# Performance work log

Hardware: AMD Instinct MI355X
Metric: run time of the kernel (lower is better)

## Reference

```python
import jax, jax.numpy as jnp
import numpy as np


def _gru(ub, lengths, W_ih, W_hh, b_ih, b_hh, h0):
    # ub: [B,T,E] pooled basket sequence; emulates packed GRU + pad_packed:
    # hidden carries forward only while t < length; outputs are zero past length.
    B, T, E = ub.shape
    x_t = jnp.transpose(ub, (1, 0, 2))                      # [T,B,E]
    mask_t = (jnp.arange(T)[:, None] < lengths[None, :])    # [T,B]
    xg_t = x_t @ W_ih.T + b_ih                              # [T,B,3E] precompute input gates

    def step(h, inp):
        xg, m = inp                                         # [B,3E], [B]
        hg = h @ W_hh.T + b_hh                              # [B,3E]
        xr, xz, xn = jnp.split(xg, 3, axis=-1)
        hr, hz, hn = jnp.split(hg, 3, axis=-1)
        r = jax.nn.sigmoid(xr + hr)
        z = jax.nn.sigmoid(xz + hz)
        n = jnp.tanh(xn + r * hn)
        h_new = (1.0 - z) * n + z * h
        m = m[:, None]
        h_next = jnp.where(m, h_new, h)
        out = jnp.where(m, h_new, 0.0)                      # pad_packed pads with zeros
        return h_next, out

    h_last, outs = jax.lax.scan(step, h0[0], (xg_t, mask_t))
    dynamic_user = jnp.transpose(outs, (1, 0, 2))           # [B,T,E]
    return dynamic_user, h_last[None]                        # h_u: [1,B,E]


def setup_inputs() -> dict:
    key = jax.random.key(0)
    B, T, M, E, V = 256, 50, 20, 128, 100000
    ks = jax.random.split(key, 8)
    basket_sizes = jax.random.randint(ks[0], (B, T), 1, M + 1)
    item_ids = jax.random.randint(ks[1], (B, T, M), 1, V + 2)
    pos = jnp.arange(M)
    item_ids = jnp.where(pos[None, None, :] < basket_sizes[..., None], item_ids, 0)
    lengths = jnp.sort(jax.random.randint(ks[2], (B,), 1, T + 1))[::-1]  # descending, like pack_padded
    emb = jax.random.normal(ks[3], (V + 2, E), jnp.float32) * 0.1
    emb = emb.at[0].set(0.0)                                 # padding_idx=0
    s = 1.0 / np.sqrt(E)
    W_ih = jax.random.uniform(ks[4], (3 * E, E), jnp.float32, -s, s)
    W_hh = jax.random.uniform(ks[5], (3 * E, E), jnp.float32, -s, s)
    b_ih = jax.random.uniform(ks[6], (3 * E,), jnp.float32, -s, s)
    b_hh = jax.random.uniform(ks[7], (3 * E,), jnp.float32, -s, s)
    h0 = jnp.zeros((1, B, E), jnp.float32)
    return {"item_ids": item_ids, "basket_sizes": basket_sizes, "lengths": lengths,
            "emb": emb, "W_ih": W_ih, "W_hh": W_hh, "b_ih": b_ih, "b_hh": b_hh, "h0": h0}


def reference(item_ids, basket_sizes, lengths, emb, W_ih, W_hh, b_ih, b_hh, h0):
    # Fused ragged embedding-bag (avg): row 0 of emb is zero, so padded slots
    # contribute nothing; divide by true basket size -> exact avg pool over basket.
    gathered = emb[item_ids]                                 # [B,T,M,E]
    ub_seqs = gathered.sum(axis=2) / basket_sizes[..., None].astype(gathered.dtype)  # [B,T,E]
    dynamic_user, h_u = _gru(ub_seqs, lengths, W_ih, W_hh, b_ih, b_hh, h0)
    return dynamic_user, h_u
```

## Files before the change

kernel.cpp:

```cpp
#include <hip/hip_runtime.h>
#include <stdint.h>

#define Bn 256
#define Tn 50
#define Mn 20
#define En 128
#define G3 384
#define MT 64
#define LDA 132

typedef float f32x4 __attribute__((ext_vector_type(4)));

__device__ __forceinline__ float sigmoidf(float x) {
    return 1.0f / (1.0f + __expf(-x));
}
__device__ __forceinline__ float tanh_safe(float a) {
    float ax = fabsf(a);
    float e2 = __expf(-2.0f * ax);
    return copysignf((1.0f - e2) / (1.0f + e2), a);
}

__device__ __forceinline__ float quad_reduce_add(float x) {
    int t1 = __builtin_amdgcn_update_dpp(0, __float_as_int(x),
                                         0xB1 , 0xF, 0xF, true);
    x += __int_as_float(t1);
    int t2 = __builtin_amdgcn_update_dpp(0, __float_as_int(x),
                                         0x4E , 0xF, 0xF, true);
    x += __int_as_float(t2);
    return x;
}

__global__ __launch_bounds__(256) void gather_kernel(
    const int*   __restrict__ item_ids,
    const int*   __restrict__ basket_sizes,
    const float* __restrict__ emb,
    float* __restrict__ ub)
{
    const int bt   = blockIdx.x * 8 + (threadIdx.x >> 5);
    const int lane = threadIdx.x & 31;
    const int* ids = item_ids + (size_t)bt * Mn;
    float ax = 0.f, ay = 0.f, az = 0.f, aw = 0.f;
    #pragma unroll
    for (int m = 0; m < Mn; ++m) {
        const float4 v = *(const float4*)(emb + (size_t)ids[m] * En + lane * 4);
        ax += v.x; ay += v.y; az += v.z; aw += v.w;
    }
    const float inv = 1.0f / (float)basket_sizes[bt];
    *(float4*)(ub + (size_t)bt * En + lane * 4) =
        make_float4(ax * inv, ay * inv, az * inv, aw * inv);
}

__global__ __launch_bounds__(256, 2) void gemm_kernel(
    const float* __restrict__ ub,
    const float* __restrict__ W_ih,
    const float* __restrict__ b_ih,
    float* __restrict__ xg)
{
    __shared__ float A[MT][LDA];
    __shared__ float Bt[64][LDA];

    const int tid  = threadIdx.x;
    const int mt   = blockIdx.x / 6;
    const int nc   = blockIdx.x % 6;
    const int row0 = mt * MT;
    const int col0 = nc * 64;

    {
        const int r = tid >> 2, seg = tid & 3;
        const float4* srcA = (const float4*)(ub + (size_t)(row0 + r) * En + seg * 32);
        const float4* srcB = (const float4*)(W_ih + (size_t)(col0 + r) * En + seg * 32);
        float4* dstA = (float4*)&A[r][seg * 32];
        float4* dstB = (float4*)&Bt[r][seg * 32];
        #pragma unroll
        for (int c = 0; c < 8; ++c) { dstA[c] = srcA[c]; dstB[c] = srcB[c]; }
    }
    __syncthreads();

    const int tx = tid & 15;
    const int ty = tid >> 4;

    float acc[4][4];
    #pragma unroll
    for (int i = 0; i < 4; ++i)
        #pragma unroll
        for (int u = 0; u < 4; ++u) acc[i][u] = 0.0f;

    #pragma unroll 4
    for (int k4 = 0; k4 < 32; ++k4) {
        const float4 av[4] = {
            *(const float4*)&A[ty +  0][k4*4], *(const float4*)&A[ty + 16][k4*4],
            *(const float4*)&A[ty + 32][k4*4], *(const float4*)&A[ty + 48][k4*4]};
        const float4 bv[4] = {
            *(const float4*)&Bt[tx +  0][k4*4], *(const float4*)&Bt[tx + 16][k4*4],
            *(const float4*)&Bt[tx + 32][k4*4], *(const float4*)&Bt[tx + 48][k4*4]};
        #pragma unroll
        for (int i = 0; i < 4; ++i)
            #pragma unroll
            for (int u = 0; u < 4; ++u) {
                acc[i][u] = fmaf(av[i].x, bv[u].x, acc[i][u]);
                acc[i][u] = fmaf(av[i].y, bv[u].y, acc[i][u]);
                acc[i][u] = fmaf(av[i].z, bv[u].z, acc[i][u]);
                acc[i][u] = fmaf(av[i].w, bv[u].w, acc[i][u]);
            }
    }

    float bias[4];
    #pragma unroll
    for (int u = 0; u < 4; ++u) bias[u] = b_ih[col0 + tx + 16*u];
    #pragma unroll
    for (int i = 0; i < 4; ++i) {
        const size_t rowoff = (size_t)(row0 + ty + 16*i) * G3;
        #pragma unroll
        for (int u = 0; u < 4; ++u)
            xg[rowoff + col0 + tx + 16*u] = acc[i][u] + bias[u];
    }
}

__global__ __launch_bounds__(512) void gru_kernel(
    const int*   __restrict__ lengths,
    const float* __restrict__ W_hh,
    const float* __restrict__ b_hh,
    const float* __restrict__ h0,
    const float* __restrict__ xg,
    float* __restrict__ out_dyn,
    float* __restrict__ out_h)
{
    extern __shared__ float smem[];
    float* hs  = smem;
    float* sxg = smem + 2 * En;

    const int tid = threadIdx.x;
    const int b   = blockIdx.x;
    const int j   = tid >> 2;
    const int q   = tid & 3;

    const int len = lengths[b];
    const float* xgb = xg + (size_t)b * Tn * G3;
    float* outb = out_dyn + (size_t)b * Tn * En;

    {
        const float4* src = (const float4*)xgb;
        float4* dst = (float4*)sxg;
        const int nv4 = len * (G3 / 4);
        for (int i = tid; i < nv4; i += 512) dst[i] = src[i];
    }

    f32x4 w0[8], w1[8], w2[8];
    {
        const f32x4* p0 = (const f32x4*)(W_hh + (size_t)(0*En + j) * En + q * 32);
        const f32x4* p1 = (const f32x4*)(W_hh + (size_t)(1*En + j) * En + q * 32);
        const f32x4* p2 = (const f32x4*)(W_hh + (size_t)(2*En + j) * En + q * 32);
        #pragma unroll
        for (int c = 0; c < 8; ++c) {
            const int cc = (c + 2*q) & 7;
            w0[c] = p0[cc]; w1[c] = p1[cc]; w2[c] = p2[cc];
        }
    }

    const float br = b_hh[j], bz = b_hh[En + j], bn = b_hh[2*En + j];
    float hprev = h0[(size_t)b * En + j];
    if (q == 0) hs[j] = hprev;
    __syncthreads();

    int cur = 0;
    for (int t = 0; t < len; ++t) {
        const float x0r = sxg[t*G3 + j];
        const float x0z = sxg[t*G3 + En + j];
        const float x0n = sxg[t*G3 + 2*En + j];

        const f32x4* h4 = ((const f32x4*)(hs + cur * En)) + q * 8;
        float a0 = 0.f, a1 = 0.f, a2 = 0.f;
        #pragma unroll
        for (int c = 0; c < 8; ++c) {
            const f32x4 hv = h4[(c + 2*q) & 7];
            a0 = fmaf(w0[c].x, hv.x, a0); a0 = fmaf(w0[c].y, hv.y, a0);
            a0 = fmaf(w0[c].z, hv.z, a0); a0 = fmaf(w0[c].w, hv.w, a0);
            a1 = fmaf(w1[c].x, hv.x, a1); a1 = fmaf(w1[c].y, hv.y, a1);
            a1 = fmaf(w1[c].z, hv.z, a1); a1 = fmaf(w1[c].w, hv.w, a1);
            a2 = fmaf(w2[c].x, hv.x, a2); a2 = fmaf(w2[c].y, hv.y, a2);
            a2 = fmaf(w2[c].z, hv.z, a2); a2 = fmaf(w2[c].w, hv.w, a2);
        }

        a0 = quad_reduce_add(a0);
        a1 = quad_reduce_add(a1);
        a2 = quad_reduce_add(a2);

        const float r = sigmoidf(x0r + br + a0);
        const float z = sigmoidf(x0z + bz + a1);
        const float n = tanh_safe(x0n + r * (bn + a2));
        const float hnew = (1.0f - z) * n + z * hprev;

        if (q == 0) {
            hs[(cur ^ 1) * En + j] = hnew;
            outb[t*En + j] = hnew;
        }
        asm volatile("s_waitcnt lgkmcnt(0)" ::: "memory");
        __builtin_amdgcn_s_barrier();
        __builtin_amdgcn_sched_barrier(0);

        hprev = hnew;
        cur ^= 1;
    }

    if (q == 0) {
        for (int t = len; t < Tn; ++t) outb[t*En + j] = 0.0f;
        out_h[(size_t)b * En + j] = hprev;
    }
}

extern "C" void kernel_launch(void* const* d_in, const int* in_sizes, int n_in,
                              void* d_out, int out_size, void* d_ws, size_t ws_size,
                              hipStream_t stream) {
    const int*   item_ids     = (const int*)d_in[0];
    const int*   basket_sizes = (const int*)d_in[1];
    const int*   lengths      = (const int*)d_in[2];
    const float* emb          = (const float*)d_in[3];
    const float* W_ih         = (const float*)d_in[4];
    const float* W_hh         = (const float*)d_in[5];
    const float* b_ih         = (const float*)d_in[6];
    const float* b_hh         = (const float*)d_in[7];
    const float* h0           = (const float*)d_in[8];
    float* out = (float*)d_out;
    float* xg  = (float*)d_ws;
    float* ub  = out;

    static bool lds_attr_set = false;
    if (!lds_attr_set) {
        (void)hipFuncSetAttribute((const void*)gru_kernel,
                                  hipFuncAttributeMaxDynamicSharedMemorySize,
                                  (2 * En + Tn * G3) * (int)sizeof(float));
        lds_attr_set = true;
    }

    gather_kernel<<<(Bn * Tn) / 8, 256, 0, stream>>>(item_ids, basket_sizes, emb, ub);
    gemm_kernel<<<1200, 256, 0, stream>>>(ub, W_ih, b_ih, xg);
    gru_kernel<<<Bn, 512, (2 * En + Tn * G3) * sizeof(float), stream>>>(
        lengths, W_hh, b_hh, h0, xg, out, out + (size_t)Bn * Tn * En);
}
```

Before: 174.1 us.

## Split GRU hidden dot products across two lanes instead of four

The GRU recurrence now uses 256 threads per batch row, with two lanes per hidden unit instead of four. Each lane holds 64 columns of each of the three W_hh gate rows in registers (192 floats), and the cross-lane reduction shrinks to a single DPP step. The aim is to cut the per-step reduction and barrier cost, since a block is now 4 waves rather than 8. In exchange, each lane runs a serial FMA chain twice as long, the register footprint grows sharply, and the bank-conflict staggering on the hidden-state LDS reads is removed.

```diff
diff --git a/kernel.cpp b/kernel.cpp
--- a/kernel.cpp
+++ b/kernel.cpp
@@ -18,16 +18,6 @@
     float ax = fabsf(a);
     float e2 = __expf(-2.0f * ax);
     return copysignf((1.0f - e2) / (1.0f + e2), a);
-}
-
-__device__ __forceinline__ float quad_reduce_add(float x) {
-    int t1 = __builtin_amdgcn_update_dpp(0, __float_as_int(x),
-                                         0xB1 , 0xF, 0xF, true);
-    x += __int_as_float(t1);
-    int t2 = __builtin_amdgcn_update_dpp(0, __float_as_int(x),
-                                         0x4E , 0xF, 0xF, true);
-    x += __int_as_float(t2);
-    return x;
 }
 
 __global__ __launch_bounds__(256) void gather_kernel(
@@ -116,7 +106,7 @@
     }
 }
 
-__global__ __launch_bounds__(512) void gru_kernel(
+__global__ __launch_bounds__(256, 1) void gru_kernel(
     const int*   __restrict__ lengths,
     const float* __restrict__ W_hh,
     const float* __restrict__ b_hh,
@@ -131,8 +121,8 @@
 
     const int tid = threadIdx.x;
     const int b   = blockIdx.x;
-    const int j   = tid >> 2;
-    const int q   = tid & 3;
+    const int j   = tid >> 1;
+    const int s   = tid & 1;
 
     const int len = lengths[b];
     const float* xgb = xg + (size_t)b * Tn * G3;
@@ -142,24 +132,21 @@
         const float4* src = (const float4*)xgb;
         float4* dst = (float4*)sxg;
         const int nv4 = len * (G3 / 4);
-        for (int i = tid; i < nv4; i += 512) dst[i] = src[i];
-    }
-
-    f32x4 w0[8], w1[8], w2[8];
+        for (int i = tid; i < nv4; i += 256) dst[i] = src[i];
+    }
+
+    f32x4 w0[16], w1[16], w2[16];
     {
-        const f32x4* p0 = (const f32x4*)(W_hh + (size_t)(0*En + j) * En + q * 32);
-        const f32x4* p1 = (const f32x4*)(W_hh + (size_t)(1*En + j) * En + q * 32);
-        const f32x4* p2 = (const f32x4*)(W_hh + (size_t)(2*En + j) * En + q * 32);
-        #pragma unroll
-        for (int c = 0; c < 8; ++c) {
-            const int cc = (c + 2*q) & 7;
-            w0[c] = p0[cc]; w1[c] = p1[cc]; w2[c] = p2[cc];
-        }
+        const f32x4* p0 = (const f32x4*)(W_hh + (size_t)(0*En + j) * En + s * 64);
+        const f32x4* p1 = (const f32x4*)(W_hh + (size_t)(1*En + j) * En + s * 64);
+        const f32x4* p2 = (const f32x4*)(W_hh + (size_t)(2*En + j) * En + s * 64);
+        #pragma unroll
+        for (int c = 0; c < 16; ++c) { w0[c] = p0[c]; w1[c] = p1[c]; w2[c] = p2[c]; }
     }
 
     const float br = b_hh[j], bz = b_hh[En + j], bn = b_hh[2*En + j];
     float hprev = h0[(size_t)b * En + j];
-    if (q == 0) hs[j] = hprev;
+    if (s == 0) hs[j] = hprev;
     __syncthreads();
 
     int cur = 0;
@@ -168,11 +155,11 @@
         const float x0z = sxg[t*G3 + En + j];
         const float x0n = sxg[t*G3 + 2*En + j];
 
-        const f32x4* h4 = ((const f32x4*)(hs + cur * En)) + q * 8;
+        const f32x4* h4 = ((const f32x4*)(hs + cur * En)) + s * 16;
         float a0 = 0.f, a1 = 0.f, a2 = 0.f;
         #pragma unroll
-        for (int c = 0; c < 8; ++c) {
-            const f32x4 hv = h4[(c + 2*q) & 7];
+        for (int c = 0; c < 16; ++c) {
+            const f32x4 hv = h4[c];
             a0 = fmaf(w0[c].x, hv.x, a0); a0 = fmaf(w0[c].y, hv.y, a0);
             a0 = fmaf(w0[c].z, hv.z, a0); a0 = fmaf(w0[c].w, hv.w, a0);
             a1 = fmaf(w1[c].x, hv.x, a1); a1 = fmaf(w1[c].y, hv.y, a1);
@@ -181,16 +168,24 @@
             a2 = fmaf(w2[c].z, hv.z, a2); a2 = fmaf(w2[c].w, hv.w, a2);
         }
 
-        a0 = quad_reduce_add(a0);
-        a1 = quad_reduce_add(a1);
-        a2 = quad_reduce_add(a2);
+        {
+            int t0 = __builtin_amdgcn_update_dpp(0, __float_as_int(a0),
+                                                 0xB1, 0xF, 0xF, true);
+            a0 += __int_as_float(t0);
+            int u0 = __builtin_amdgcn_update_dpp(0, __float_as_int(a1),
+                                                 0xB1, 0xF, 0xF, true);
+            a1 += __int_as_float(u0);
+            int v0 = __builtin_amdgcn_update_dpp(0, __float_as_int(a2),
+                                                 0xB1, 0xF, 0xF, true);
+            a2 += __int_as_float(v0);
+        }
 
         const float r = sigmoidf(x0r + br + a0);
         const float z = sigmoidf(x0z + bz + a1);
         const float n = tanh_safe(x0n + r * (bn + a2));
         const float hnew = (1.0f - z) * n + z * hprev;
 
-        if (q == 0) {
+        if (s == 0) {
             hs[(cur ^ 1) * En + j] = hnew;
             outb[t*En + j] = hnew;
         }
@@ -202,7 +197,7 @@
         cur ^= 1;
     }
 
-    if (q == 0) {
+    if (s == 0) {
         for (int t = len; t < Tn; ++t) outb[t*En + j] = 0.0f;
         out_h[(size_t)b * En + j] = hprev;
     }
@@ -234,6 +229,6 @@
 
     gather_kernel<<<(Bn * Tn) / 8, 256, 0, stream>>>(item_ids, basket_sizes, emb, ub);
     gemm_kernel<<<1200, 256, 0, stream>>>(ub, W_ih, b_ih, xg);
-    gru_kernel<<<Bn, 512, (2 * En + Tn * G3) * sizeof(float), stream>>>(
+    gru_kernel<<<Bn, 256, (2 * En + Tn * G3) * sizeof(float), stream>>>(
         lengths, W_hh, b_hh, h0, xg, out, out + (size_t)Bn * Tn * En);
 }
```

New measurement: 180.3 us. 1.04x slower.
